# Performance work log

Measured on AMD Instinct MI355X. Metric: run time of the kernel, lower is better.

The kernel has to match this reference:

```python
import jax, jax.numpy as jnp
import numpy as np
import math

TAU = 1.0          # args.gumbel_tau, used as GMM variance scale in assign()
RD = 64            # args.reduce_dimension
NE = 8             # args.dynamic_nexperts
COMMIT = 0.1       # args.commitment_scale
T, B, C, O = 2048, 8, 512, 512


def setup_inputs() -> dict:
    key = jax.random.key(0)
    ks = jax.random.split(key, 9)
    a = math.sqrt(6.0) / (C + O)  # init for pw_w per dynamic_init_method==1
    return {
        "x": jax.random.normal(ks[0], (T, B, C), jnp.float32),
        "key_feat": jax.random.normal(ks[1], (T, B, C), jnp.float32),  # ignored by forward
        "map_w": jax.random.normal(ks[2], (RD, C), jnp.float32) * math.sqrt(2.0 / (C + RD)),
        "map_b": jnp.zeros((RD,), jnp.float32),
        "centroids": jax.random.normal(ks[3], (NE, RD), jnp.float32) * 0.02,
        "prior": jnp.ones((1, NE), jnp.float32) / NE,
        "pw_w": jax.random.uniform(ks[4], (NE, O * C), jnp.float32, -a, a),
        "bias_w": jax.random.normal(ks[5], (O, C), jnp.float32) * 0.02,
        "bias_b": jnp.zeros((O,), jnp.float32),
    }


def reference(x, key_feat, map_w, map_b, centroids, prior, pw_w, bias_w, bias_b):
    # x: [T, B, C] time-major. key_feat is ignored, matching the original forward.
    Tq, Bq, Cq = x.shape
    N = Tq * Bq
    xf = x.reshape(N, Cq)
    # GMM key projection: [N, RD]
    k = xf @ map_w.T + map_b
    # squared euclid distance to centroids: [N, NE]
    d2 = (jnp.sum(k * k, axis=1, keepdims=True)
          + jnp.sum(centroids * centroids, axis=1)[None, :]
          - 2.0 * (k @ centroids.T))
    # soft GMM responsibilities (training path, no gumbel sampling)
    logresp = (-0.5 * TAU * d2
               - (RD / 2.0) * math.log(2.0 * math.pi * TAU)
               + jnp.log(prior))                                  # [N, NE]
    denom = jax.scipy.special.logsumexp(logresp, axis=-1, keepdims=True)
    resp = jnp.exp(logresp - denom)                               # [N, NE]
    loss = COMMIT * (-jnp.sum(denom))
    # Expert mixture. Original: w = (resp @ pw_w).reshape(T,B,O,C); y = w @ x.
    # Same math, fused order: apply each expert to x, then mix with resp.
    W = pw_w.reshape(NE, O, Cq)
    z = jnp.einsum('ni,eoi->neo', xf, W)        # [N, NE, O] per-expert outputs
    y = jnp.einsum('ne,neo->no', resp, z)       # [N, O]
    y = y.reshape(Tq, Bq, O)
    # dynamic bias: Linear(key_dim -> O) applied to x0
    y = y + x @ bias_w.T + bias_b
    return y, loss
```

## Files before the change

### kernel.cpp

```cpp
#include <hip/hip_runtime.h>
#include <hip/hip_bf16.h>

#define NROWS 16384
#define CC 512
#define OO 512
#define RDIM 64
#define NE 8
#define NEXP 9
#define COMMIT_SCALE 0.1f
#define LOG2PI_TERM 58.81206612509905f

typedef __attribute__((ext_vector_type(8))) short short8;
typedef __attribute__((ext_vector_type(4))) float f32x4;

__device__ __forceinline__ unsigned short f2bf(float f) {
  unsigned int u = __float_as_uint(f);
  u += 0x7fffu + ((u >> 16) & 1u);
  return (unsigned short)(u >> 16);
}
__device__ __forceinline__ unsigned int pk2(float a, float b) {
  return ((unsigned int)f2bf(a)) | (((unsigned int)f2bf(b)) << 16);
}

__device__ __forceinline__ void gl_lds16(const unsigned short* g, unsigned short* l) {
  __builtin_amdgcn_global_load_lds(
      (const __attribute__((address_space(1))) void*)g,
      (__attribute__((address_space(3))) void*)l, 16, 0, 0);
}

#define P4 524288u
#define B4 65536u
#define NCV ((P4 + B4) / 256u)
#define TB 128u

__global__ __launch_bounds__(256) void k_prep(
    const float* __restrict__ pw, const float* __restrict__ bw,
    const float* __restrict__ mw,
    unsigned short* __restrict__ wb, float* __restrict__ wT4)
{
  unsigned int b = blockIdx.x;
  if (b >= NCV) {
    unsigned int i = (b - NCV) * 256 + threadIdx.x;
    unsigned int j = i >> 9, c = i & 511u;
    wT4[((c >> 2) << 8) + (j << 2) + (c & 3u)] = mw[i];
    return;
  }
  unsigned int i = b * 256 + threadIdx.x;
  const float* src = (i < P4) ? (pw + (size_t)i * 4)
                              : (bw + (size_t)(i - P4) * 4);
  unsigned short* dst = wb + (size_t)i * 4;
  float4 v = *(const float4*)src;
  ushort4 o;
  o.x = f2bf(v.x); o.y = f2bf(v.y); o.z = f2bf(v.z); o.w = f2bf(v.w);
  *(ushort4*)dst = o;
}

__global__ __launch_bounds__(256) void k_assign(
    const float* __restrict__ x,
    const float* __restrict__ wT4,
    const float* __restrict__ map_b,
    const float* __restrict__ cent,
    const float* __restrict__ prior,
    float* __restrict__ resp_out,
    float* __restrict__ loss_acc)
{
  __shared__ float lsum[4];
  const int tid  = threadIdx.x;
  const int wid  = tid >> 6;
  const int lane = tid & 63;
  const int row0 = blockIdx.x * 16 + wid * 4;

  const float* xr0 = x + (size_t)row0 * CC;
  float acc[4] = {0.f, 0.f, 0.f, 0.f};
  #pragma unroll 4
  for (int c0 = 0; c0 < CC; c0 += 4) {
    float4 wv = *(const float4*)&wT4[(c0 << 6) + (lane << 2)];
    #pragma unroll
    for (int r = 0; r < 4; ++r) {
      float4 xv = *(const float4*)(xr0 + r * CC + c0);
      acc[r] += xv.x * wv.x + xv.y * wv.y + xv.z * wv.z + xv.w * wv.w;
    }
  }
  const float mb = map_b[lane];
  float kk[4] = {acc[0] + mb, acc[1] + mb, acc[2] + mb, acc[3] + mb};

  float ce[8], c2[8], lp[8];
  #pragma unroll
  for (int e = 0; e < 8; ++e) {
    ce[e] = cent[e * RDIM + lane];
    float v = ce[e] * ce[e];
    #pragma unroll
    for (int off = 32; off; off >>= 1) v += __shfl_xor(v, off, 64);
    c2[e] = v;
    lp[e] = __logf(prior[e]);
  }

  float dsum = 0.f;
  #pragma unroll
  for (int r = 0; r < 4; ++r) {
    float k = kk[r];
    float v[9];
    v[0] = k * k;
    #pragma unroll
    for (int e = 0; e < 8; ++e) v[e + 1] = k * ce[e];
    #pragma unroll
    for (int off = 32; off; off >>= 1) {
      #pragma unroll
      for (int q = 0; q < 9; ++q) v[q] += __shfl_xor(v[q], off, 64);
    }
    float lr[8], mx = -3.4e38f;
    #pragma unroll
    for (int e = 0; e < 8; ++e) {
      float d2 = v[0] + c2[e] - 2.f * v[e + 1];
      lr[e] = -0.5f * d2 - LOG2PI_TERM + lp[e];
      mx = fmaxf(mx, lr[e]);
    }
    float s = 0.f;
    #pragma unroll
    for (int e = 0; e < 8; ++e) s += __expf(lr[e] - mx);
    float denom = mx + __logf(s);
    dsum += denom;
    float myv = 0.f;
    #pragma unroll
    for (int e = 0; e < 8; ++e) {
      float re = __expf(lr[e] - denom);
      myv = (lane == e) ? re : myv;
    }
    if (lane < 8) resp_out[(size_t)(row0 + r) * NE + lane] = myv;
  }
  if (lane == 0) lsum[wid] = dsum;
  __syncthreads();
  if (tid == 0) {
    float t = lsum[0] + lsum[1] + lsum[2] + lsum[3];
    atomicAdd(loss_acc, -COMMIT_SCALE * t);
  }
}

__global__ __launch_bounds__(256, 3) void k_moe(
    const float* __restrict__ x,
    const unsigned short* __restrict__ wb,
    const float* __restrict__ bb,
    const float* __restrict__ resp,
    const float* __restrict__ loss_acc,
    float* __restrict__ out)
{
  __shared__ unsigned short aT[128 * 40];
  __shared__ unsigned short bT[128 * 32];
  __shared__ float sc[NEXP * 128];

  const int tid = threadIdx.x;
  const int m0 = blockIdx.x * 128;
  const int o0 = blockIdx.y * 128;

  for (int idx = tid; idx < 128 * NE; idx += 256) {
    int r = idx >> 3, e = idx & 7;
    sc[e * 128 + r] = resp[(size_t)(m0 + r) * NE + e];
  }
  if (tid < 128) sc[8 * 128 + tid] = 1.0f;
  __syncthreads();

  const int lane = tid & 63;
  const int wid = tid >> 6;
  const int wm = (wid & 1) * 64;
  const int wn = (wid >> 1) * 64;
  const int fr = lane & 15;
  const int fq = lane >> 4;

  const int srow = tid >> 1;
  const int scol = (tid & 1) * 16;
  const float4* xr4 = (const float4*)(x + (size_t)(m0 + srow) * CC + scol);

  const int srB = lane >> 2;
  const int gchunk = (lane & 3) ^ (srB & 3) ^ ((srB >> 2) & 3);
  const size_t b_go = (size_t)(o0 + wid * 32 + srB) * CC + gchunk * 8;
  unsigned short* b_l0 = bT + wid * 1024;
  unsigned short* b_l1 = b_l0 + 512;
  const size_t row16 = (size_t)16 * CC;
  const int rchunkB = (fq ^ (fr & 3) ^ ((fr >> 2) & 3)) * 8;

  f32x4 zero4 = {0.f, 0.f, 0.f, 0.f};
  f32x4 acc[4][4];
  #pragma unroll
  for (int i = 0; i < 4; ++i)
    #pragma unroll
    for (int j = 0; j < 4; ++j) acc[i][j] = zero4;

  for (int e = 0; e < NEXP; ++e) {
    const unsigned short* Bb = wb + (size_t)e * OO * CC + b_go;
    const float s = sc[e * 128 + srow];

    #pragma unroll 2
    for (int kk = 0; kk < 16; ++kk) {
      __syncthreads();
      gl_lds16(Bb + kk * 32,         b_l0);
      gl_lds16(Bb + kk * 32 + row16, b_l1);
      float4 v0 = xr4[kk * 8 + 0], v1 = xr4[kk * 8 + 1];
      float4 v2 = xr4[kk * 8 + 2], v3 = xr4[kk * 8 + 3];
      uint4 w0, w1;
      w0.x = pk2(v0.x * s, v0.y * s); w0.y = pk2(v0.z * s, v0.w * s);
      w0.z = pk2(v1.x * s, v1.y * s); w0.w = pk2(v1.z * s, v1.w * s);
      w1.x = pk2(v2.x * s, v2.y * s); w1.y = pk2(v2.z * s, v2.w * s);
      w1.z = pk2(v3.x * s, v3.y * s); w1.w = pk2(v3.z * s, v3.w * s);
      *(uint4*)&aT[srow * 40 + scol]     = w0;
      *(uint4*)&aT[srow * 40 + scol + 8] = w1;
      __syncthreads();

      short8 af[4], bfr[4];
      #pragma unroll
      for (int i = 0; i < 4; ++i)
        af[i] = *(const short8*)&aT[(wm + i * 16 + fr) * 40 + fq * 8];
      #pragma unroll
      for (int j = 0; j < 4; ++j)
        bfr[j] = *(const short8*)&bT[(wn + j * 16 + fr) * 32 + rchunkB];

      #pragma unroll
      for (int i = 0; i < 4; ++i)
        #pragma unroll
        for (int j = 0; j < 4; ++j)
          acc[i][j] = __builtin_amdgcn_mfma_f32_16x16x32_bf16(af[i], bfr[j], acc[i][j], 0, 0, 0);
    }
  }

  #pragma unroll
  for (int j = 0; j < 4; ++j) {
    const int o = o0 + wn + j * 16 + fr;
    const float bias = bb[o];
    #pragma unroll
    for (int i = 0; i < 4; ++i) {
      #pragma unroll
      for (int r = 0; r < 4; ++r) {
        int m = m0 + wm + i * 16 + fq * 4 + r;
        out[(size_t)m * OO + o] = acc[i][j][r] + bias;
      }
    }
  }

  if (blockIdx.x == 0 && blockIdx.y == 0 && tid == 0)
    out[(size_t)NROWS * OO] = loss_acc[0];
}

extern "C" void kernel_launch(void* const* d_in, const int* in_sizes, int n_in,
                              void* d_out, int out_size, void* d_ws, size_t ws_size,
                              hipStream_t stream) {
  const float* x     = (const float*)d_in[0];
  const float* map_w = (const float*)d_in[2];
  const float* map_b = (const float*)d_in[3];
  const float* cent  = (const float*)d_in[4];
  const float* prior = (const float*)d_in[5];
  const float* pw    = (const float*)d_in[6];
  const float* bw    = (const float*)d_in[7];
  const float* bb    = (const float*)d_in[8];
  float* out = (float*)d_out;

  char* wsp = (char*)d_ws;
  float* resp = (float*)wsp;
  float* loss = (float*)(wsp + 524288);
  unsigned short* wb = (unsigned short*)(wsp + 524304);
  float* wT4 = (float*)(wsp + 524304 + 4718592);

  hipMemsetAsync(loss, 0, sizeof(float), stream);
  k_prep<<<dim3(NCV + TB), dim3(256), 0, stream>>>(pw, bw, map_w, wb, wT4);
  k_assign<<<dim3(NROWS / 16), dim3(256), 0, stream>>>(x, wT4, map_b, cent, prior, resp, loss);
  dim3 grid(NROWS / 128, OO / 128);
  k_moe<<<grid, dim3(256), 0, stream>>>(x, wb, bb, resp, loss, out);
}
```

Baseline: 366.0 us.

## Double-buffer LDS tiles and prefetch x registers in MoE GEMM loop

Flattens the expert and k loops into a single 144-iteration loop and double-buffers the A and B LDS tiles. Each iteration now has one barrier, and the next tile's global-to-LDS loads and the scaled bf16 packing overlap the current MFMA work. x rows are prefetched two iterations ahead into registers. The cost is twice the LDS and more registers, and the occupancy hint drops from 3 to 2 blocks per CU.

```diff
diff --git a/kernel.cpp b/kernel.cpp
--- a/kernel.cpp
+++ b/kernel.cpp
@@ -7,6 +7,7 @@
 #define RDIM 64
 #define NE 8
 #define NEXP 9
+#define KITER 144
 #define COMMIT_SCALE 0.1f
 #define LOG2PI_TERM 58.81206612509905f
 
@@ -136,7 +137,7 @@
   }
 }
 
-__global__ __launch_bounds__(256, 3) void k_moe(
+__global__ __launch_bounds__(256, 2) void k_moe(
     const float* __restrict__ x,
     const unsigned short* __restrict__ wb,
     const float* __restrict__ bb,
@@ -144,8 +145,8 @@
     const float* __restrict__ loss_acc,
     float* __restrict__ out)
 {
-  __shared__ unsigned short aT[128 * 40];
-  __shared__ unsigned short bT[128 * 32];
+  __shared__ unsigned short aT[2][128 * 40];
+  __shared__ unsigned short bT[2][128 * 32];
   __shared__ float sc[NEXP * 128];
 
   const int tid = threadIdx.x;
@@ -157,7 +158,6 @@
     sc[e * 128 + r] = resp[(size_t)(m0 + r) * NE + e];
   }
   if (tid < 128) sc[8 * 128 + tid] = 1.0f;
-  __syncthreads();
 
   const int lane = tid & 63;
   const int wid = tid >> 6;
@@ -168,14 +168,14 @@
 
   const int srow = tid >> 1;
   const int scol = (tid & 1) * 16;
-  const float4* xr4 = (const float4*)(x + (size_t)(m0 + srow) * CC + scol);
+  const float4* xbase = (const float4*)(x + (size_t)(m0 + srow) * CC) + (tid & 1) * 4;
 
   const int srB = lane >> 2;
   const int gchunk = (lane & 3) ^ (srB & 3) ^ ((srB >> 2) & 3);
   const size_t b_go = (size_t)(o0 + wid * 32 + srB) * CC + gchunk * 8;
-  unsigned short* b_l0 = bT + wid * 1024;
-  unsigned short* b_l1 = b_l0 + 512;
+  const unsigned short* wbp = wb + b_go;
   const size_t row16 = (size_t)16 * CC;
+  const int ldsB = wid * 1024;
   const int rchunkB = (fq ^ (fr & 3) ^ ((fr >> 2) & 3)) * 8;
 
   f32x4 zero4 = {0.f, 0.f, 0.f, 0.f};
@@ -185,40 +185,66 @@
     #pragma unroll
     for (int j = 0; j < 4; ++j) acc[i][j] = zero4;
 
-  for (int e = 0; e < NEXP; ++e) {
-    const unsigned short* Bb = wb + (size_t)e * OO * CC + b_go;
-    const float s = sc[e * 128 + srow];
-
-    #pragma unroll 2
-    for (int kk = 0; kk < 16; ++kk) {
-      __syncthreads();
-      gl_lds16(Bb + kk * 32,         b_l0);
-      gl_lds16(Bb + kk * 32 + row16, b_l1);
-      float4 v0 = xr4[kk * 8 + 0], v1 = xr4[kk * 8 + 1];
-      float4 v2 = xr4[kk * 8 + 2], v3 = xr4[kk * 8 + 3];
+  float4 xr[2][4];
+  __syncthreads();
+
+  #pragma unroll
+  for (int t = 0; t < 4; ++t) xr[0][t] = xbase[t];
+  {
+    const float s = sc[srow];
+    uint4 w0, w1;
+    w0.x = pk2(xr[0][0].x * s, xr[0][0].y * s); w0.y = pk2(xr[0][0].z * s, xr[0][0].w * s);
+    w0.z = pk2(xr[0][1].x * s, xr[0][1].y * s); w0.w = pk2(xr[0][1].z * s, xr[0][1].w * s);
+    w1.x = pk2(xr[0][2].x * s, xr[0][2].y * s); w1.y = pk2(xr[0][2].z * s, xr[0][2].w * s);
+    w1.z = pk2(xr[0][3].x * s, xr[0][3].y * s); w1.w = pk2(xr[0][3].z * s, xr[0][3].w * s);
+    *(uint4*)&aT[0][srow * 40 + scol]     = w0;
+    *(uint4*)&aT[0][srow * 40 + scol + 8] = w1;
+  }
+  gl_lds16(wbp,         &bT[0][ldsB]);
+  gl_lds16(wbp + row16, &bT[0][ldsB + 512]);
+  #pragma unroll
+  for (int t = 0; t < 4; ++t) xr[1][t] = xbase[8 + t];
+
+  #pragma unroll 2
+  for (int it = 0; it < KITER; ++it) {
+    const int cur = it & 1, nxt = cur ^ 1;
+    __syncthreads();
+
+    short8 af[4], bfr[4];
+    #pragma unroll
+    for (int i = 0; i < 4; ++i)
+      af[i] = *(const short8*)&aT[cur][(wm + i * 16 + fr) * 40 + fq * 8];
+    #pragma unroll
+    for (int j = 0; j < 4; ++j)
+      bfr[j] = *(const short8*)&bT[cur][(wn + j * 16 + fr) * 32 + rchunkB];
+
+    if (it < KITER - 1) {
+      const int it1 = it + 1;
+      const unsigned short* Bb = wbp + (size_t)(it1 >> 4) * (OO * CC) + (it1 & 15) * 32;
+      gl_lds16(Bb,         &bT[nxt][ldsB]);
+      gl_lds16(Bb + row16, &bT[nxt][ldsB + 512]);
+      const float s = sc[(it1 >> 4) * 128 + srow];
+      const float4 v0 = xr[it1 & 1][0], v1 = xr[it1 & 1][1];
+      const float4 v2 = xr[it1 & 1][2], v3 = xr[it1 & 1][3];
       uint4 w0, w1;
       w0.x = pk2(v0.x * s, v0.y * s); w0.y = pk2(v0.z * s, v0.w * s);
       w0.z = pk2(v1.x * s, v1.y * s); w0.w = pk2(v1.z * s, v1.w * s);
       w1.x = pk2(v2.x * s, v2.y * s); w1.y = pk2(v2.z * s, v2.w * s);
       w1.z = pk2(v3.x * s, v3.y * s); w1.w = pk2(v3.z * s, v3.w * s);
-      *(uint4*)&aT[srow * 40 + scol]     = w0;
-      *(uint4*)&aT[srow * 40 + scol + 8] = w1;
-      __syncthreads();
-
-      short8 af[4], bfr[4];
-      #pragma unroll
-      for (int i = 0; i < 4; ++i)
-        af[i] = *(const short8*)&aT[(wm + i * 16 + fr) * 40 + fq * 8];
+      *(uint4*)&aT[nxt][srow * 40 + scol]     = w0;
+      *(uint4*)&aT[nxt][srow * 40 + scol + 8] = w1;
+      if (it < KITER - 2) {
+        const int k2 = (it + 2) & 15;
+        #pragma unroll
+        for (int t = 0; t < 4; ++t) xr[cur][t] = xbase[k2 * 8 + t];
+      }
+    }
+
+    #pragma unroll
+    for (int i = 0; i < 4; ++i)
       #pragma unroll
       for (int j = 0; j < 4; ++j)
-        bfr[j] = *(const short8*)&bT[(wn + j * 16 + fr) * 32 + rchunkB];
-
-      #pragma unroll
-      for (int i = 0; i < 4; ++i)
-        #pragma unroll
-        for (int j = 0; j < 4; ++j)
-          acc[i][j] = __builtin_amdgcn_mfma_f32_16x16x32_bf16(af[i], bfr[j], acc[i][j], 0, 0, 0);
-    }
+        acc[i][j] = __builtin_amdgcn_mfma_f32_16x16x32_bf16(af[i], bfr[j], acc[i][j], 0, 0, 0);
   }
 
   #pragma unroll
```

Result: slower. 584.1 us (+59.6%).
